# Kernel optimization log

Hardware: AMD Instinct MI355X
Metric: run time of the kernel (lower is better)

## Reference

```python
import jax, jax.numpy as jnp
from jax import lax
import numpy as np

FSIZE = 5
NUM_FILTERS = 8


def setup_inputs() -> dict:
    key = jax.random.key(0)
    k1, k2, k3 = jax.random.split(key, 3)
    B, H, W = 8, 1024, 1024
    scale = 1.0 / (FSIZE * FSIZE)  # matches .normal_(0, 1/(fsize*fsize))
    return {
        "mosaick": jax.random.uniform(k1, (B, 1, H, W), dtype=jnp.float32),
        "sel_filts": jax.random.normal(k2, (NUM_FILTERS, FSIZE, FSIZE), dtype=jnp.float32) * scale,
        "green_filts": jax.random.normal(k3, (NUM_FILTERS, FSIZE, FSIZE), dtype=jnp.float32) * scale,
    }


def _conv_bank(x_padded, filts):
    # x_padded: [B,1,H+2p,W+2p], filts: [K,f,f] -> [B,K,H,W]
    return lax.conv_general_dilated(
        x_padded, filts[:, None, :, :], (1, 1), "VALID",
        dimension_numbers=("NCHW", "OIHW", "NCHW"))


def reference(mosaick, sel_filts, green_filts):
    # Space-variant learned demosaicking of the green channel:
    # per-pixel softmax over a bank of selection-filter responses picks a
    # convex combination of candidate green interpolations; known green
    # samples (GRBG: x%2 == y%2) are passed through from the mosaick.
    B, _, H, W = mosaick.shape
    p = FSIZE // 2
    padded = jnp.pad(mosaick, ((0, 0), (0, 0), (p, p), (p, p)), mode="edge")
    sel = _conv_bank(padded, sel_filts)        # [B,K,H,W] selection scores
    interp = _conv_bank(padded, green_filts)   # [B,K,H,W] green candidates
    w = jax.nn.softmax(sel, axis=1)            # per-pixel filter weights
    green_hat = jnp.sum(w * interp, axis=1, keepdims=True)  # [B,1,H,W]
    yy = jnp.arange(H)[:, None]
    xx = jnp.arange(W)[None, :]
    gmask = ((xx % 2) == (yy % 2)).astype(mosaick.dtype)  # GRBG green sites
    green = gmask * mosaick + (1.0 - gmask) * green_hat
    return green  # corresponds to output[:, 1:2, ...]
```

## Files before the change

### kernel.cpp

```cpp
#include <hip/hip_runtime.h>

#define HH 1024
#define WW 1024

typedef __fp16 h2 __attribute__((ext_vector_type(2)));

__global__ __launch_bounds__(256, 2)
void demosaick_kernel(const float* __restrict__ mosaick,
                      const float* __restrict__ sel_filts,
                      const float* __restrict__ green_filts,
                      float* __restrict__ out) {
    __shared__ h2 filt2[15 * 16];

    const int tid = threadIdx.y * 64 + threadIdx.x;
    if (tid < 240) {
        int ch = tid & 15;
        int t  = tid >> 4;
        int dy = t / 3;
        int pr = t - dy * 3;
        int dx0 = 2 * pr;
        const float* src = (ch < 8) ? sel_filts : green_filts;
        int base = (ch & 7) * 25 + dy * 5 + dx0;
        float v0 = src[base];
        float v1 = (dx0 + 1 < 5) ? src[base + 1] : 0.f;
        filt2[tid] = __builtin_amdgcn_cvt_pkrtz(v0, v1);
    }
    __syncthreads();

    const int b  = blockIdx.z;
    const int y0 = blockIdx.y * 16 + threadIdx.y * 4;
    const int x0 = (blockIdx.x * 64 + threadIdx.x) * 2;
    const float* img = mosaick + (size_t)b * (HH * WW);

    h2 hE[8][3];
    h2 hO[8][3];
    float cen[4];
    #pragma unroll
    for (int j = 0; j < 8; ++j) {
        int r = y0 + j - 2;
        r = r < 0 ? 0 : (r > HH - 1 ? HH - 1 : r);
        const float* rp = img + (size_t)r * WW;
        float w[6];
        #pragma unroll
        for (int i = 0; i < 6; ++i) {
            int c = x0 + i - 2;
            c = c < 0 ? 0 : (c > WW - 1 ? WW - 1 : c);
            w[i] = rp[c];
        }
        hE[j][0] = __builtin_amdgcn_cvt_pkrtz(w[0], w[1]);
        hE[j][1] = __builtin_amdgcn_cvt_pkrtz(w[2], w[3]);
        hE[j][2] = __builtin_amdgcn_cvt_pkrtz(w[4], 0.f);
        hO[j][0] = __builtin_amdgcn_cvt_pkrtz(w[1], w[2]);
        hO[j][1] = __builtin_amdgcn_cvt_pkrtz(w[3], w[4]);
        hO[j][2] = __builtin_amdgcn_cvt_pkrtz(w[5], 0.f);
        if (j >= 2 && j <= 5)
            cen[j - 2] = ((j - 2) & 1) ? w[3] : w[2];
    }

    float accS[4][8];
    #pragma unroll
    for (int p = 0; p < 4; ++p)
        #pragma unroll
        for (int c = 0; c < 8; ++c) accS[p][c] = 0.f;

    #pragma unroll
    for (int dy = 0; dy < 5; ++dy) {
        #pragma unroll
        for (int pr = 0; pr < 3; ++pr) {
            const h2* fp = &filt2[(dy * 3 + pr) * 16];
            h2 f[8];
            #pragma unroll
            for (int c = 0; c < 8; ++c) f[c] = fp[c];
            #pragma unroll
            for (int p = 0; p < 4; ++p) {
                h2 wp = (p & 1) ? hE[p + dy][pr] : hO[p + dy][pr];
                #pragma unroll
                for (int c = 0; c < 8; ++c)
                    accS[p][c] = __builtin_amdgcn_fdot2(wp, f[c], accS[p][c], false);
            }
        }
    }

    const float L2E = 1.44269504f;
    float sum[4], gh[4];
    #pragma unroll
    for (int p = 0; p < 4; ++p) {
        float m = accS[p][0];
        #pragma unroll
        for (int c = 1; c < 8; ++c) m = fmaxf(m, accS[p][c]);
        float mL = m * L2E;
        float s = 0.f;
        #pragma unroll
        for (int c = 0; c < 8; ++c) {
            float e = __builtin_amdgcn_exp2f(fmaf(accS[p][c], L2E, -mL));
            accS[p][c] = e;
            s += e;
        }
        sum[p] = s;
        gh[p] = 0.f;
    }

    #pragma unroll
    for (int hlf = 0; hlf < 2; ++hlf) {
        float accG[4][4];
        #pragma unroll
        for (int p = 0; p < 4; ++p)
            #pragma unroll
            for (int c = 0; c < 4; ++c) accG[p][c] = 0.f;

        #pragma unroll
        for (int dy = 0; dy < 5; ++dy) {
            #pragma unroll
            for (int pr = 0; pr < 3; ++pr) {
                const h2* fp = &filt2[(dy * 3 + pr) * 16 + 8 + 4 * hlf];
                h2 f[4];
                #pragma unroll
                for (int c = 0; c < 4; ++c) f[c] = fp[c];
                #pragma unroll
                for (int p = 0; p < 4; ++p) {
                    h2 wp = (p & 1) ? hE[p + dy][pr] : hO[p + dy][pr];
                    #pragma unroll
                    for (int c = 0; c < 4; ++c)
                        accG[p][c] = __builtin_amdgcn_fdot2(wp, f[c], accG[p][c], false);
                }
            }
        }
        #pragma unroll
        for (int p = 0; p < 4; ++p)
            #pragma unroll
            for (int c = 0; c < 4; ++c)
                gh[p] = fmaf(accS[p][4 * hlf + c], accG[p][c], gh[p]);
    }

    float* outp = out + (size_t)b * (HH * WW);
    #pragma unroll
    for (int p = 0; p < 4; ++p) {
        float g = gh[p] * __builtin_amdgcn_rcpf(sum[p]);
        float2 o;
        if ((p & 1) == 0) { o.x = cen[p]; o.y = g; }
        else              { o.x = g;      o.y = cen[p]; }
        *(float2*)(outp + (size_t)(y0 + p) * WW + x0) = o;
    }
}

extern "C" void kernel_launch(void* const* d_in, const int* in_sizes, int n_in,
                              void* d_out, int out_size, void* d_ws, size_t ws_size,
                              hipStream_t stream) {
    const float* mosaick     = (const float*)d_in[0];
    const float* sel_filts   = (const float*)d_in[1];
    const float* green_filts = (const float*)d_in[2];
    float* out = (float*)d_out;
    const int HW = HH * WW;
    const int B = in_sizes[0] / HW;
    dim3 grid(WW / 128, HH / 16, B);
    dim3 block(64, 4, 1);
    hipLaunchKernelGGL(demosaick_kernel, grid, block, 0, stream,
                       mosaick, sel_filts, green_filts, out);
}
```

Measured before the change: 119.2 us.

## Stage block input tile as packed half pairs in shared memory

Each block now cooperatively loads its 20x132 haloed input region once, converts it to even- and odd-aligned fp16 pairs, and stores them in LDS. Threads then read their 8x3 packed window registers from LDS instead of issuing 48 clamped global loads each. The passthrough centre sample is reloaded from global at store time in full precision. This cuts redundant global and L1 traffic between neighbouring threads, at the cost of an extra staging loop, a barrier, and about 10 KB of LDS per block.

```diff
diff --git a/kernel.cpp b/kernel.cpp
--- a/kernel.cpp
+++ b/kernel.cpp
@@ -10,9 +10,16 @@
                       const float* __restrict__ sel_filts,
                       const float* __restrict__ green_filts,
                       float* __restrict__ out) {
+    __shared__ h2 E2[20][66];
+    __shared__ h2 O2[20][66];
     __shared__ h2 filt2[15 * 16];
 
     const int tid = threadIdx.y * 64 + threadIdx.x;
+    const int b   = blockIdx.z;
+    const int by0 = blockIdx.y * 16;
+    const int bx0 = blockIdx.x * 128;
+    const float* img = mosaick + (size_t)b * (HH * WW);
+
     if (tid < 240) {
         int ch = tid & 15;
         int t  = tid >> 4;
@@ -25,36 +32,37 @@
         float v1 = (dx0 + 1 < 5) ? src[base + 1] : 0.f;
         filt2[tid] = __builtin_amdgcn_cvt_pkrtz(v0, v1);
     }
+
+    for (int idx = tid; idx < 20 * 66; idx += 256) {
+        int r = idx / 66;
+        int k = idx - r * 66;
+        int gy = by0 - 2 + r;
+        gy = gy < 0 ? 0 : (gy > HH - 1 ? HH - 1 : gy);
+        const float* rp = img + (size_t)gy * WW;
+        int g0 = bx0 - 2 + 2 * k;
+        int c0 = g0 < 0 ? 0 : (g0 > WW - 1 ? WW - 1 : g0);
+        int c1 = g0 + 1 < 0 ? 0 : (g0 + 1 > WW - 1 ? WW - 1 : g0 + 1);
+        int c2 = g0 + 2 < 0 ? 0 : (g0 + 2 > WW - 1 ? WW - 1 : g0 + 2);
+        float f0 = rp[c0], f1 = rp[c1], f2 = rp[c2];
+        E2[r][k] = __builtin_amdgcn_cvt_pkrtz(f0, f1);
+        O2[r][k] = __builtin_amdgcn_cvt_pkrtz(f1, f2);
+    }
     __syncthreads();
 
-    const int b  = blockIdx.z;
-    const int y0 = blockIdx.y * 16 + threadIdx.y * 4;
-    const int x0 = (blockIdx.x * 64 + threadIdx.x) * 2;
-    const float* img = mosaick + (size_t)b * (HH * WW);
+    const int lx = threadIdx.x;
+    const int y0 = by0 + threadIdx.y * 4;
+    const int x0 = bx0 + lx * 2;
 
     h2 hE[8][3];
     h2 hO[8][3];
-    float cen[4];
     #pragma unroll
     for (int j = 0; j < 8; ++j) {
-        int r = y0 + j - 2;
-        r = r < 0 ? 0 : (r > HH - 1 ? HH - 1 : r);
-        const float* rp = img + (size_t)r * WW;
-        float w[6];
+        int r = threadIdx.y * 4 + j;
         #pragma unroll
-        for (int i = 0; i < 6; ++i) {
-            int c = x0 + i - 2;
-            c = c < 0 ? 0 : (c > WW - 1 ? WW - 1 : c);
-            w[i] = rp[c];
+        for (int pr = 0; pr < 3; ++pr) {
+            hE[j][pr] = E2[r][lx + pr];
+            hO[j][pr] = O2[r][lx + pr];
         }
-        hE[j][0] = __builtin_amdgcn_cvt_pkrtz(w[0], w[1]);
-        hE[j][1] = __builtin_amdgcn_cvt_pkrtz(w[2], w[3]);
-        hE[j][2] = __builtin_amdgcn_cvt_pkrtz(w[4], 0.f);
-        hO[j][0] = __builtin_amdgcn_cvt_pkrtz(w[1], w[2]);
-        hO[j][1] = __builtin_amdgcn_cvt_pkrtz(w[3], w[4]);
-        hO[j][2] = __builtin_amdgcn_cvt_pkrtz(w[5], 0.f);
-        if (j >= 2 && j <= 5)
-            cen[j - 2] = ((j - 2) & 1) ? w[3] : w[2];
     }
 
     float accS[4][8];
@@ -135,10 +143,11 @@
     float* outp = out + (size_t)b * (HH * WW);
     #pragma unroll
     for (int p = 0; p < 4; ++p) {
+        float cen = img[(size_t)(y0 + p) * WW + x0 + (p & 1)];
         float g = gh[p] * __builtin_amdgcn_rcpf(sum[p]);
         float2 o;
-        if ((p & 1) == 0) { o.x = cen[p]; o.y = g; }
-        else              { o.x = g;      o.y = cen[p]; }
+        if ((p & 1) == 0) { o.x = cen; o.y = g; }
+        else              { o.x = g;   o.y = cen; }
         *(float2*)(outp + (size_t)(y0 + p) * WW + x0) = o;
     }
 }
```

Measured after the change: 121.5 us. About the same (+1.9%).
